# Optimization experiments

Measured on AMD Instinct MI355X. Metric: run time of the kernel, lower is better.

## Reference

```python
import jax, jax.numpy as jnp
import numpy as np

B, F, Q, E = 256, 128, 4096, 128
TAU = 0.2
P_DROP = 0.5
NUM_SAMPLES = 128  # hardcoded in forward: compute_scores(..., num_samples=128)
NUM_POS = 1
EASY_UB = 0.5
HARD_LB = 0.5


def setup_inputs() -> dict:
    k = jax.random.key(0)
    ks = jax.random.split(k, 8)
    query = jax.random.normal(ks[0], (B, F), jnp.float32)
    key = jax.random.normal(ks[1], (B, F), jnp.float32)
    teacher = jax.random.normal(ks[2], (B, F), jnp.float32)
    negatives = jax.random.normal(ks[3], (F, Q), jnp.float32)
    # random_maskout masks: rand <= p -> zero out
    mask_t = jax.random.uniform(ks[4], (E, B, F)) <= P_DROP
    mask_n = jax.random.uniform(ks[5], (E, F, Q)) <= P_DROP
    # compute_scores sampling mask: rand <= num_samples/Q
    score_mask = jax.random.uniform(ks[6], (E, B, Q)) <= (NUM_SAMPLES / Q)
    # bootstrap over batch dim: for each (e,q) column, sample B row indices with replacement
    idx = jax.random.randint(ks[7], (E, Q, B), 0, B)
    boot = jnp.zeros((E, Q, B), bool).at[
        jnp.arange(E)[:, None, None], jnp.arange(Q)[None, :, None], idx
    ].set(True)
    boot_mask = jnp.transpose(boot, (0, 2, 1))  # (E,B,Q)
    return dict(query=query, key=key, teacher=teacher, negatives=negatives,
                mask_t=mask_t, mask_n=mask_n, score_mask=score_mask, boot_mask=boot_mask)


def _masked_softmax(x, mask, axis):
    # matches torch masked_fill(~mask, -inf) + softmax; masked entries -> 0 prob
    z = jnp.where(mask, x, -jnp.inf)
    m = jnp.max(z, axis=axis, keepdims=True)
    m = jnp.where(jnp.isfinite(m), m, 0.0)  # guard fully-masked slices
    e = jnp.where(mask, jnp.exp(z - m), 0.0)
    return e / jnp.maximum(e.sum(axis=axis, keepdims=True), 1e-30)


def _l2norm(x, axis):
    n = jnp.sqrt(jnp.sum(x * x, axis=axis, keepdims=True))
    return x / jnp.maximum(n, 1e-12)


def reference(query, key, teacher, negatives, mask_t, mask_n, score_mask, boot_mask):
    negatives = jax.lax.stop_gradient(negatives)  # negatives.detach().clone()
    logits_pos = jnp.sum(query * key, axis=1, keepdims=True)      # (B,1)
    logits_neg = query @ negatives                                 # (B,Q)
    logits = jnp.concatenate([logits_pos, logits_neg], axis=1) / TAU
    moco_loss = -jax.nn.log_softmax(logits, axis=1)[:, 0].mean()   # CE with target 0

    # ---- teacher similarities (torch.no_grad) ----
    t = _l2norm(jnp.where(mask_t, 0.0, teacher[None, :, :]), 2)    # (E,B,F)
    n = _l2norm(jnp.where(mask_n, 0.0, negatives[None, :, :]), 1)  # (E,F,Q)
    sim = jax.lax.stop_gradient(jnp.einsum('ebf,efq->ebq', t, n) / TAU)

    # ---- scores: masked softmax over Q, masked mean over E ----
    probs = _masked_softmax(sim, score_mask, axis=2)               # (E,B,Q)
    cnt_e = jnp.maximum(score_mask.sum(axis=0).astype(sim.dtype), 1.0)
    scores = probs.sum(axis=0) / cnt_e                             # (B,Q)

    # ---- uncertainty: masked entropy over batch dim ----
    p = _masked_softmax(sim, boot_mask, axis=1) + 1e-7             # (E,B,Q)
    ent = -(p * jnp.log(p))
    cnt_b = jnp.maximum(boot_mask.sum(axis=1).astype(sim.dtype), 1.0)  # (E,Q)
    uncertainty = (ent.sum(axis=1) / cnt_b).mean(axis=0, keepdims=True)  # (1,Q)

    log_sm_neg = jax.nn.log_softmax(logits[:, 1:], axis=1)         # (B,Q)

    def _pos_loss(pos_mask_row):
        pm = jnp.broadcast_to(pos_mask_row, (B, Q))
        s = jnp.where(pm, scores, -jnp.inf)
        _, idx = jax.lax.top_k(s, NUM_POS)                         # (B,k)
        loss = -jnp.take_along_axis(log_sm_neg, idx, axis=1).mean(axis=1).mean()
        mask = jnp.zeros((B, Q), bool).at[jnp.arange(B)[:, None], idx].set(True)
        return loss, mask

    ub = jnp.quantile(uncertainty, EASY_UB, axis=1)                # (1,)
    easy_loss, easy_mask = _pos_loss(uncertainty <= ub)
    lb = jnp.quantile(uncertainty, HARD_LB, axis=1)
    hard_loss, hard_mask = _pos_loss(uncertainty >= lb)

    return moco_loss, logits, easy_loss, easy_mask, hard_loss, hard_mask
```

## Files before the change

### kernel.cpp

```cpp
#include <hip/hip_runtime.h>
#include <cmath>

typedef unsigned char u8;
typedef unsigned short u16;
typedef unsigned int u32;
typedef __attribute__((ext_vector_type(8))) short s8v;
typedef __attribute__((ext_vector_type(4))) float f32x4;

#define B 256
#define F 128
#define Q 4096
#define E 128
#define QW 128
#define INV_TAU 5.0f
#define CAP 256

#define W_SCORES 0u
#define W_CNT    1048576u
#define W_UNC    2097152u
#define W_NLSE   2101248u
#define W_MOCO   2101504u
#define W_EASY   2101760u
#define W_HARD   2102016u
#define W_UB     2102272u
#define W_INVN   2102528u
#define W_AF     2626816u
#define W_PB     4723968u
#define W_PS     8918272u
#define W_PN     13112576u
#define W_CNTB   15209728u
#define W_ENT    15242496u

#define O_MOCO   0u
#define O_LOGITS 1u
#define O_ELOSS  1048833u
#define O_EMASK  1048834u
#define O_HLOSS  2097410u
#define O_HMASK  2097411u

static __device__ __forceinline__ u16 f2bf(float x) {
    unsigned int u = __builtin_bit_cast(unsigned int, x);
    unsigned int r = (u + 0x7FFFu + ((u >> 16) & 1u)) >> 16;
    return (u16)r;
}

__global__ void k_zero(float4* __restrict__ p) {
    p[(size_t)blockIdx.x * 256 + threadIdx.x] = make_float4(0.f, 0.f, 0.f, 0.f);
}
__global__ void k_zeroi(int* __restrict__ p) {
    p[(size_t)blockIdx.x * 256 + threadIdx.x] = 0;
}

__global__ void __launch_bounds__(256) k_pack(const u8* __restrict__ in,
                                              u32* __restrict__ out, int Rin) {
    __shared__ u32 lds[64 * 133];
    int t = threadIdx.x;
    int r0 = blockIdx.x * 64;
    int q0 = blockIdx.y * 512;
    int qw0 = q0 >> 5;
    #pragma unroll
    for (int i = 0; i < 8; i++) {
        int w = i * 256 + t;
        int row = w >> 5, c = w & 31;
        uint4 v = *(const uint4*)&in[(size_t)(r0 + row) * Q + q0 + c * 16];
        int base = row * 133 + c * 4;
        lds[base] = v.x; lds[base + 1] = v.y; lds[base + 2] = v.z; lds[base + 3] = v.w;
    }
    __syncthreads();
    int e = r0 / Rin, rr = r0 % Rin;
    #pragma unroll
    for (int k = 0; k < 4; k++) {
        int qw = (t >> 6) + k * 4;
        int r = t & 63;
        u32 w = 0;
        #pragma unroll
        for (int j = 0; j < 8; j++) {
            u32 u = lds[r * 133 + qw * 8 + j];
            w |= ((u & 1u) | ((u >> 7) & 2u) | ((u >> 14) & 4u) | ((u >> 21) & 8u)) << (j * 4);
        }
        out[((size_t)e * QW + qw0 + qw) * Rin + rr + r] = w;
    }
}

__global__ void k_afrag(const float* __restrict__ teacher, const u8* __restrict__ mask_t,
                        u16* __restrict__ af) {
    int eb = blockIdx.x;
    int e  = eb >> 8;
    int b  = eb & (B - 1);
    int f  = threadIdx.x;
    float v = mask_t[(size_t)eb * F + f] ? 0.f : teacher[b * F + f];
    float ss = v * v;
    #pragma unroll
    for (int o = 32; o > 0; o >>= 1) ss += __shfl_down(ss, o);
    __shared__ float s2[2];
    if ((threadIdx.x & 63) == 0) s2[threadIdx.x >> 6] = ss;
    __syncthreads();
    float d = fmaxf(sqrtf(s2[0] + s2[1]), 1e-12f);
    float t = v / d;
    int bg = b >> 4, m = b & 15;
    int kb = f >> 5, quad = (f >> 3) & 3, j = f & 7;
    int lane = quad * 16 + m;
    af[((((size_t)e * 16 + bg) * 4 + kb) * 64 + lane) * 8 + j] = f2bf(t);
}

__global__ void __launch_bounds__(256) k_invn(const float* __restrict__ neg,
                                              const u32* __restrict__ pn,
                                              float* __restrict__ invn) {
    __shared__ u32 lds[32 * 128];
    int e = blockIdx.x, t = threadIdx.x;
    int qblk = blockIdx.y;
    size_t base = ((size_t)e * QW + qblk * 32) * F;
    #pragma unroll
    for (int k = 0; k < 16; k++) lds[t + 256 * k] = pn[base + t + 256 * k];
    __syncthreads();
    int q0 = qblk * 1024 + t * 4;
    int qwl = (t * 4) >> 5;
    int sh = (t * 4) & 31;
    float s0 = 0.f, s1 = 0.f, s2 = 0.f, s3 = 0.f;
    #pragma unroll 4
    for (int f = 0; f < F; f++) {
        float4 v = *(const float4*)&neg[(size_t)f * Q + q0];
        u32 w = lds[qwl * 128 + f] >> sh;
        if (!(w & 1u)) s0 = fmaf(v.x, v.x, s0);
        if (!(w & 2u)) s1 = fmaf(v.y, v.y, s1);
        if (!(w & 4u)) s2 = fmaf(v.z, v.z, s2);
        if (!(w & 8u)) s3 = fmaf(v.w, v.w, s3);
    }
    float4 r;
    r.x = INV_TAU / fmaxf(sqrtf(s0), 1e-12f);
    r.y = INV_TAU / fmaxf(sqrtf(s1), 1e-12f);
    r.z = INV_TAU / fmaxf(sqrtf(s2), 1e-12f);
    r.w = INV_TAU / fmaxf(sqrtf(s3), 1e-12f);
    *(float4*)&invn[(size_t)e * Q + q0] = r;
}

__global__ void __launch_bounds__(256) k_fused(
        const u16* __restrict__ af, const float* __restrict__ neg,
        const u32* __restrict__ pn, const float* __restrict__ invn,
        const u32* __restrict__ pb, const u32* __restrict__ ps,
        float* __restrict__ unc, uint2* __restrict__ ent_buf,
        int* __restrict__ cnt_buf, int e0) {
    __shared__ u16 bfrag[4][4][512];
    __shared__ u32 bw[2][256], sw[2][256];
    __shared__ u32 pnl[2][128];
    __shared__ float invl[64];
    __shared__ float sstat[4][64], cstat[4][64], estat[4][64];
    __shared__ float carr[64];
    __shared__ int sbase[256];

    int qb = blockIdx.x;
    int el = blockIdx.y, e = e0 + el;
    int t = threadIdx.x;
    int q0 = qb * 64;
    int qw0 = qb * 2;

    bw[0][t] = pb[((size_t)e * QW + qw0) * B + t];
    bw[1][t] = pb[((size_t)e * QW + qw0 + 1) * B + t];
    sw[0][t] = ps[((size_t)e * QW + qw0) * B + t];
    sw[1][t] = ps[((size_t)e * QW + qw0 + 1) * B + t];
    if (t < 128) {
        pnl[0][t] = pn[((size_t)e * QW + qw0) * F + t];
        pnl[1][t] = pn[((size_t)e * QW + qw0 + 1) * F + t];
    } else if (t < 192) {
        invl[t - 128] = invn[(size_t)e * Q + q0 + (t - 128)];
    }
    __syncthreads();

    #pragma unroll
    for (int s = 0; s < 4; s++) {
        int slot = t + 256 * s;
        int qg = slot >> 8;
        int r = slot & 255;
        int kb = r >> 6, lane2 = r & 63;
        int ql = qg * 16 + (lane2 & 15);
        int fb = kb * 32 + (lane2 >> 4) * 8;
        float iv = invl[ql];
        const u32* pw = pnl[ql >> 5];
        int sh = ql & 31;
        u16 tmp[8];
        #pragma unroll
        for (int j = 0; j < 8; j++) {
            u32 bit = (pw[fb + j] >> sh) & 1u;
            float v = bit ? 0.f : neg[(size_t)(fb + j) * Q + q0 + ql] * iv;
            tmp[j] = f2bf(v);
        }
        *(s8v*)&bfrag[qg][kb][lane2 * 8] = *(const s8v*)tmp;
    }
    __syncthreads();

    int wave = t >> 6, lane = t & 63;
    int colb = lane & 15, quad = lane >> 4;
    f32x4 acc[4][4];
    #pragma unroll
    for (int bgi = 0; bgi < 4; bgi++) {
        int bg = wave * 4 + bgi;
        s8v a[4];
        #pragma unroll
        for (int kb = 0; kb < 4; kb++)
            a[kb] = *(const s8v*)&af[((((size_t)e * 16 + bg) * 4 + kb) * 64 + lane) * 8];
        #pragma unroll
        for (int qg = 0; qg < 4; qg++) {
            f32x4 c4 = {0.f, 0.f, 0.f, 0.f};
            #pragma unroll
            for (int kb = 0; kb < 4; kb++) {
                s8v bv = *(const s8v*)&bfrag[qg][kb][lane * 8];
                c4 = __builtin_amdgcn_mfma_f32_16x16x32_bf16(a[kb], bv, c4, 0, 0, 0);
            }
            acc[bgi][qg] = c4;
        }
    }

    float sloc[4] = {0.f, 0.f, 0.f, 0.f}, cloc[4] = {0.f, 0.f, 0.f, 0.f};
    #pragma unroll
    for (int bgi = 0; bgi < 4; bgi++) {
        int b0 = (wave * 4 + bgi) * 16 + quad * 4;
        uint4 w0 = *(const uint4*)&bw[0][b0];
        uint4 w1 = *(const uint4*)&bw[1][b0];
        u32 W0[4] = {w0.x, w0.y, w0.z, w0.w};
        u32 W1[4] = {w1.x, w1.y, w1.z, w1.w};
        #pragma unroll
        for (int r = 0; r < 4; r++)
            #pragma unroll
            for (int qg = 0; qg < 4; qg++) {
                u32 w = (qg & 2) ? W1[r] : W0[r];
                int bpos = (qg & 1) * 16 + colb;
                if ((w >> bpos) & 1u) {
                    sloc[qg] += __expf(acc[bgi][qg][r]);
                    cloc[qg] += 1.f;
                }
            }
    }
    #pragma unroll
    for (int qg = 0; qg < 4; qg++) {
        sloc[qg] += __shfl_xor(sloc[qg], 16); sloc[qg] += __shfl_xor(sloc[qg], 32);
        cloc[qg] += __shfl_xor(cloc[qg], 16); cloc[qg] += __shfl_xor(cloc[qg], 32);
    }
    if (quad == 0)
        #pragma unroll
        for (int qg = 0; qg < 4; qg++) {
            sstat[wave][qg * 16 + colb] = sloc[qg];
            cstat[wave][qg * 16 + colb] = cloc[qg];
        }
    __syncthreads();
    float invS[4];
    #pragma unroll
    for (int qg = 0; qg < 4; qg++) {
        int c = qg * 16 + colb;
        float S = sstat[0][c] + sstat[1][c] + sstat[2][c] + sstat[3][c];
        invS[qg] = 1.f / fmaxf(S, 1e-30f);
    }
    if (wave == 0 && quad == 0)
        #pragma unroll
        for (int qg = 0; qg < 4; qg++) {
            int c = qg * 16 + colb;
            carr[c] = cstat[0][c] + cstat[1][c] + cstat[2][c] + cstat[3][c];
        }

    const float P0 = 1e-7f;
    const float C0 = 1.61180954e-6f;
    float eloc[4] = {0.f, 0.f, 0.f, 0.f};
    #pragma unroll
    for (int bgi = 0; bgi < 4; bgi++) {
        int b0 = (wave * 4 + bgi) * 16 + quad * 4;
        uint4 w0 = *(const uint4*)&bw[0][b0];
        uint4 w1 = *(const uint4*)&bw[1][b0];
        u32 W0[4] = {w0.x, w0.y, w0.z, w0.w};
        u32 W1[4] = {w1.x, w1.y, w1.z, w1.w};
        #pragma unroll
        for (int r = 0; r < 4; r++)
            #pragma unroll
            for (int qg = 0; qg < 4; qg++) {
                u32 w = (qg & 2) ? W1[r] : W0[r];
                int bpos = (qg & 1) * 16 + colb;
                if ((w >> bpos) & 1u) {
                    float p = __expf(acc[bgi][qg][r]) * invS[qg] + P0;
                    eloc[qg] -= p * __logf(p);
                } else {
                    eloc[qg] += C0;
                }
            }
    }
    #pragma unroll
    for (int qg = 0; qg < 4; qg++) {
        eloc[qg] += __shfl_xor(eloc[qg], 16); eloc[qg] += __shfl_xor(eloc[qg], 32);
    }
    if (quad == 0)
        #pragma unroll
        for (int qg = 0; qg < 4; qg++) estat[wave][qg * 16 + colb] = eloc[qg];

    {
        u32 a0 = sw[0][t], a1 = sw[1][t];
        int n = __popc(a0) + __popc(a1);
        int base = 0;
        if (n) base = atomicAdd(&cnt_buf[el * B + t], n);
        sbase[t] = base;
    }
    __syncthreads();

    if (t < 64) {
        float tot = estat[0][t] + estat[1][t] + estat[2][t] + estat[3][t];
        atomicAdd(&unc[q0 + t], tot / fmaxf(carr[t], 1.f));
    }

    #pragma unroll
    for (int bgi = 0; bgi < 4; bgi++) {
        int b0 = (wave * 4 + bgi) * 16 + quad * 4;
        uint4 s0 = *(const uint4*)&sw[0][b0];
        uint4 s1 = *(const uint4*)&sw[1][b0];
        u32 S0[4] = {s0.x, s0.y, s0.z, s0.w};
        u32 S1[4] = {s1.x, s1.y, s1.z, s1.w};
        #pragma unroll
        for (int r = 0; r < 4; r++) {
            int bs = sbase[b0 + r];
            int p0 = __popc(S0[r]);
            #pragma unroll
            for (int qg = 0; qg < 4; qg++) {
                int bpos = (qg & 1) * 16 + colb;
                u32 w = (qg & 2) ? S1[r] : S0[r];
                if ((w >> bpos) & 1u) {
                    int rank = __popc(w & ((1u << bpos) - 1u)) + ((qg & 2) ? p0 : 0);
                    int pos = bs + rank;
                    if (pos < CAP) {
                        uint2 en;
                        en.x = (unsigned)(q0 + qg * 16 + colb);
                        en.y = __builtin_bit_cast(unsigned, acc[bgi][qg][r]);
                        ent_buf[((size_t)(el * B + b0 + r)) * CAP + pos] = en;
                    }
                }
            }
        }
    }
}

__global__ void __launch_bounds__(256) k_scores(
        const uint2* __restrict__ ent_buf, const int* __restrict__ cnt_buf,
        float* __restrict__ sacc, float* __restrict__ cacc, int ecnt) {
    __shared__ float srow[Q];
    __shared__ float crow[Q];
    int b = blockIdx.x, t = threadIdx.x;
    #pragma unroll
    for (int j = 0; j < 16; j++) { srow[t + 256 * j] = 0.f; crow[t + 256 * j] = 0.f; }
    __syncthreads();
    int wave = t >> 6, lane = t & 63;
    for (int el = wave; el < ecnt; el += 4) {
        int c = cnt_buf[el * B + b];
        if (c > CAP) c = CAP;
        if (c == 0) continue;
        const uint2* p = ent_buf + (size_t)(el * B + b) * CAP;
        uint2 ev[4]; float exv[4]; int ne = 0;
        float s = 0.f;
        for (int i = lane; i < c; i += 64) {
            ev[ne] = p[i];
            exv[ne] = __expf(__builtin_bit_cast(float, ev[ne].y));
            s += exv[ne];
            ne++;
        }
        #pragma unroll
        for (int off = 32; off > 0; off >>= 1) s += __shfl_xor(s, off);
        float iS = 1.f / fmaxf(s, 1e-30f);
        for (int k = 0; k < ne; k++) {
            atomicAdd(&srow[ev[k].x], exv[k] * iS);
            atomicAdd(&crow[ev[k].x], 1.f);
        }
    }
    __syncthreads();
    #pragma unroll
    for (int j = 0; j < 16; j++) {
        int q = t + 256 * j;
        sacc[(size_t)b * Q + q] += srow[q];
        cacc[(size_t)b * Q + q] += crow[q];
    }
}

__global__ void k_finscores(float* __restrict__ sacc, const float* __restrict__ cacc) {
    int idx = blockIdx.x * 256 + threadIdx.x;
    sacc[idx] = sacc[idx] / fmaxf(cacc[idx], 1.f);
}

__global__ void k_logits(const float* __restrict__ query, const float* __restrict__ key,
                         const float* __restrict__ neg, float* __restrict__ out) {
    __shared__ float qrow[F];
    __shared__ float red[256];
    int b = blockIdx.x, seg = blockIdx.y, t = threadIdx.x;
    if (t < F) qrow[t] = query[b * F + t];
    __syncthreads();
    int q0 = seg * 1024 + t * 4;
    float4 acc = make_float4(0.f, 0.f, 0.f, 0.f);
    for (int f = 0; f < F; f++) {
        float a = qrow[f];
        float4 v = *(const float4*)&neg[(size_t)f * Q + q0];
        acc.x = fmaf(a, v.x, acc.x);
        acc.y = fmaf(a, v.y, acc.y);
        acc.z = fmaf(a, v.z, acc.z);
        acc.w = fmaf(a, v.w, acc.w);
    }
    float* row = out + O_LOGITS + (size_t)b * (Q + 1);
    row[1 + q0]     = acc.x * INV_TAU;
    row[1 + q0 + 1] = acc.y * INV_TAU;
    row[1 + q0 + 2] = acc.z * INV_TAU;
    row[1 + q0 + 3] = acc.w * INV_TAU;
    if (seg == 0) {
        float pp = (t < F) ? qrow[t] * key[b * F + t] : 0.f;
        red[t] = pp;
        __syncthreads();
        for (int s = 128; s > 0; s >>= 1) { if (t < s) red[t] += red[t + s]; __syncthreads(); }
        if (t == 0) row[0] = red[0] * INV_TAU;
    }
}

__global__ void k_rowstats(const float* __restrict__ out, float* __restrict__ moco_part,
                           float* __restrict__ nlse) {
    __shared__ float red[256];
    int b = blockIdx.x, t = threadIdx.x;
    const float* row = out + O_LOGITS + (size_t)b * (Q + 1);
    float m = -INFINITY, mn = -INFINITY;
    for (int j = 0; j < 17; j++) {
        int i = t + 256 * j;
        if (i < Q + 1) { float zz = row[i]; m = fmaxf(m, zz); if (i >= 1) mn = fmaxf(mn, zz); }
    }
    red[t] = m; __syncthreads();
    for (int s = 128; s > 0; s >>= 1) { if (t < s) red[t] = fmaxf(red[t], red[t + s]); __syncthreads(); }
    float M = red[0]; __syncthreads();
    red[t] = mn; __syncthreads();
    for (int s = 128; s > 0; s >>= 1) { if (t < s) red[t] = fmaxf(red[t], red[t + s]); __syncthreads(); }
    float Mn = red[0]; __syncthreads();
    float s1 = 0.f, s2 = 0.f;
    for (int j = 0; j < 17; j++) {
        int i = t + 256 * j;
        if (i < Q + 1) { float zz = row[i]; s1 += expf(zz - M); if (i >= 1) s2 += expf(zz - Mn); }
    }
    red[t] = s1; __syncthreads();
    for (int s = 128; s > 0; s >>= 1) { if (t < s) red[t] += red[t + s]; __syncthreads(); }
    float S = red[0]; __syncthreads();
    red[t] = s2; __syncthreads();
    for (int s = 128; s > 0; s >>= 1) { if (t < s) red[t] += red[t + s]; __syncthreads(); }
    float Sn = red[0];
    if (t == 0) { moco_part[b] = M + logf(S) - row[0]; nlse[b] = Mn + logf(Sn); }
}

__global__ void k_median(float* __restrict__ unc, float* __restrict__ ubp) {
    __shared__ float sd[4096];
    int t = threadIdx.x;
    #pragma unroll
    for (int j = 0; j < 4; j++) {
        int q = t + 1024 * j;
        float u = unc[q] * (1.f / 128.f);
        unc[q] = u; sd[q] = u;
    }
    __syncthreads();
    for (int k = 2; k <= 4096; k <<= 1) {
        for (int j = k >> 1; j > 0; j >>= 1) {
            #pragma unroll
            for (int base = 0; base < 4; base++) {
                int i = t + 1024 * base;
                int ixj = i ^ j;
                if (ixj > i) {
                    bool up = ((i & k) == 0);
                    float x = sd[i], y = sd[ixj];
                    if ((x > y) == up) { sd[i] = y; sd[ixj] = x; }
                }
            }
            __syncthreads();
        }
    }
    if (t == 0) { float a = sd[2047], b2 = sd[2048]; ubp[0] = a + 0.5f * (b2 - a); }
}

__global__ void k_select(float* __restrict__ out, const float* __restrict__ scores,
                         const float* __restrict__ unc, const float* __restrict__ ubp,
                         const float* __restrict__ nlse, float* __restrict__ easy_part,
                         float* __restrict__ hard_part) {
    __shared__ float rv[256];
    __shared__ int ri[256];
    __shared__ int bshare;
    int b = blockIdx.x, mode = blockIdx.y, t = threadIdx.x;
    float ub = ubp[0];
    float bv = -INFINITY; int bidx = Q;
    #pragma unroll
    for (int j = 0; j < 16; j++) {
        int q = t + 256 * j;
        float u = unc[q];
        bool ok = (mode == 0) ? (u <= ub) : (u >= ub);
        if (ok) {
            float v = scores[(size_t)b * Q + q];
            if (v > bv || (v == bv && q < bidx)) { bv = v; bidx = q; }
        }
    }
    rv[t] = bv; ri[t] = bidx; __syncthreads();
    for (int s = 128; s > 0; s >>= 1) {
        if (t < s) {
            float v2 = rv[t + s]; int i2 = ri[t + s];
            if (v2 > rv[t] || (v2 == rv[t] && i2 < ri[t])) { rv[t] = v2; ri[t] = i2; }
        }
        __syncthreads();
    }
    if (t == 0) {
        int best = ri[0]; bshare = best;
        float zz = out[O_LOGITS + (size_t)b * (Q + 1) + 1 + best];
        float loss = nlse[b] - zz;
        (mode == 0 ? easy_part : hard_part)[b] = loss;
    }
    __syncthreads();
    int best = bshare;
    float* mrow = out + (mode == 0 ? O_EMASK : O_HMASK) + (size_t)b * Q;
    #pragma unroll
    for (int j = 0; j < 16; j++) { int q = t + 256 * j; mrow[q] = (q == best) ? 1.f : 0.f; }
}

__global__ void k_scalars(const float* __restrict__ moco, const float* __restrict__ easyp,
                          const float* __restrict__ hardp, float* __restrict__ out) {
    __shared__ float red[256];
    int t = threadIdx.x;
    red[t] = moco[t]; __syncthreads();
    for (int s = 128; s > 0; s >>= 1) { if (t < s) red[t] += red[t + s]; __syncthreads(); }
    if (t == 0) out[O_MOCO] = red[0] / 256.f;
    __syncthreads();
    red[t] = easyp[t]; __syncthreads();
    for (int s = 128; s > 0; s >>= 1) { if (t < s) red[t] += red[t + s]; __syncthreads(); }
    if (t == 0) out[O_ELOSS] = red[0] / 256.f;
    __syncthreads();
    red[t] = hardp[t]; __syncthreads();
    for (int s = 128; s > 0; s >>= 1) { if (t < s) red[t] += red[t + s]; __syncthreads(); }
    if (t == 0) out[O_HLOSS] = red[0] / 256.f;
}

extern "C" void kernel_launch(void* const* d_in, const int* in_sizes, int n_in,
                              void* d_out, int out_size, void* d_ws, size_t ws_size,
                              hipStream_t stream) {
    const float* query   = (const float*)d_in[0];
    const float* key     = (const float*)d_in[1];
    const float* teacher = (const float*)d_in[2];
    const float* neg     = (const float*)d_in[3];
    const u8* mask_t     = (const u8*)d_in[4];
    const u8* mask_n     = (const u8*)d_in[5];
    const u8* score_mask = (const u8*)d_in[6];
    const u8* boot_mask  = (const u8*)d_in[7];
    float* out = (float*)d_out;
    float* ws  = (float*)d_ws;

    long ws_floats = (long)(ws_size / 4);
    int Ec = (int)((ws_floats - (long)W_ENT) / (long)(B * CAP * 2));
    if (Ec > E) Ec = E;
    if (Ec < 1) Ec = 1;

    u16* af = (u16*)(ws + W_AF);
    u32* pb = (u32*)(ws + W_PB);
    u32* ps = (u32*)(ws + W_PS);
    u32* pn = (u32*)(ws + W_PN);
    int* cnt_buf = (int*)(ws + W_CNTB);
    uint2* ent_buf = (uint2*)(ws + W_ENT);

    k_zero<<<2052, 256, 0, stream>>>((float4*)(ws + W_SCORES));
    k_pack<<<dim3((E * B) / 64, Q / 512), 256, 0, stream>>>(boot_mask, pb, B);
    k_pack<<<dim3((E * B) / 64, Q / 512), 256, 0, stream>>>(score_mask, ps, B);
    k_pack<<<dim3((E * F) / 64, Q / 512), 256, 0, stream>>>(mask_n, pn, F);
    k_afrag<<<E * B, 128, 0, stream>>>(teacher, mask_t, af);
    k_invn<<<dim3(E, 4), 256, 0, stream>>>(neg, pn, ws + W_INVN);
    k_logits<<<dim3(B, 4), 256, 0, stream>>>(query, key, neg, out);
    k_rowstats<<<B, 256, 0, stream>>>(out, ws + W_MOCO, ws + W_NLSE);

    for (int e0 = 0; e0 < E; e0 += Ec) {
        int ecnt = (E - e0 < Ec) ? (E - e0) : Ec;
        k_zeroi<<<ecnt, 256, 0, stream>>>(cnt_buf);
        k_fused<<<dim3(Q / 64, ecnt), 256, 0, stream>>>(
            af, neg, pn, ws + W_INVN, pb, ps, ws + W_UNC, ent_buf, cnt_buf, e0);
        k_scores<<<B, 256, 0, stream>>>(ent_buf, cnt_buf, ws + W_SCORES, ws + W_CNT, ecnt);
    }

    k_finscores<<<(B * Q) / 256, 256, 0, stream>>>(ws + W_SCORES, ws + W_CNT);
    k_median<<<1, 1024, 0, stream>>>(ws + W_UNC, ws + W_UB);
    k_select<<<dim3(B, 2), 256, 0, stream>>>(out, ws + W_SCORES, ws + W_UNC, ws + W_UB,
                                             ws + W_NLSE, ws + W_EASY, ws + W_HARD);
    k_scalars<<<1, 256, 0, stream>>>(ws + W_MOCO, ws + W_EASY, ws + W_HARD, out);
}
```

Baseline: 1.402 ms.

## Fuse pack launches, merge logits with rowstats, precompute score softmax sums in fused kernel

New measurement: 1.501 ms. 7.1% more time.

```diff
diff --git a/kernel.cpp b/kernel.cpp
--- a/kernel.cpp
+++ b/kernel.cpp
@@ -18,18 +18,20 @@
 #define W_SCORES 0u
 #define W_CNT    1048576u
 #define W_UNC    2097152u
-#define W_NLSE   2101248u
-#define W_MOCO   2101504u
-#define W_EASY   2101760u
-#define W_HARD   2102016u
-#define W_UB     2102272u
-#define W_INVN   2102528u
-#define W_AF     2626816u
-#define W_PB     4723968u
-#define W_PS     8918272u
-#define W_PN     13112576u
-#define W_CNTB   15209728u
-#define W_ENT    15242496u
+#define W_CNTB   2101248u
+#define W_RSUM   2134016u
+#define W_NLSE   2166784u
+#define W_MOCO   2167040u
+#define W_EASY   2167296u
+#define W_HARD   2167552u
+#define W_UB     2167808u
+#define W_INVN   2168064u
+#define W_AF     2692352u
+#define W_PB     4789504u
+#define W_PS     8983808u
+#define W_PN     13178112u
+#define W_ENT    15275264u
+#define NZERO    2166784u
 
 #define O_MOCO   0u
 #define O_LOGITS 1u
@@ -47,12 +49,17 @@
 __global__ void k_zero(float4* __restrict__ p) {
     p[(size_t)blockIdx.x * 256 + threadIdx.x] = make_float4(0.f, 0.f, 0.f, 0.f);
 }
-__global__ void k_zeroi(int* __restrict__ p) {
-    p[(size_t)blockIdx.x * 256 + threadIdx.x] = 0;
-}
-
-__global__ void __launch_bounds__(256) k_pack(const u8* __restrict__ in,
-                                              u32* __restrict__ out, int Rin) {
+
+__global__ void __launch_bounds__(256) k_pack(const u8* __restrict__ boot,
+                                              const u8* __restrict__ smask,
+                                              const u8* __restrict__ maskn,
+                                              u32* __restrict__ pb, u32* __restrict__ ps,
+                                              u32* __restrict__ pn) {
+    int z = blockIdx.z;
+    int Rin = (z == 2) ? F : B;
+    if (z == 2 && blockIdx.x >= 2048) return;
+    const u8* in = (z == 0) ? boot : (z == 1) ? smask : maskn;
+    u32* out = (z == 0) ? pb : (z == 1) ? ps : pn;
     __shared__ u32 lds[64 * 133];
     int t = threadIdx.x;
     int r0 = blockIdx.x * 64;
@@ -139,7 +146,7 @@
         const u32* __restrict__ pn, const float* __restrict__ invn,
         const u32* __restrict__ pb, const u32* __restrict__ ps,
         float* __restrict__ unc, uint2* __restrict__ ent_buf,
-        int* __restrict__ cnt_buf, int e0) {
+        int* __restrict__ cnt_buf, float* __restrict__ rsum, int e0) {
     __shared__ u16 bfrag[4][4][512];
     __shared__ u32 bw[2][256], sw[2][256];
     __shared__ u32 pnl[2][128];
@@ -210,6 +217,14 @@
         }
     }
 
+    #pragma unroll
+    for (int bgi = 0; bgi < 4; bgi++)
+        #pragma unroll
+        for (int qg = 0; qg < 4; qg++)
+            #pragma unroll
+            for (int r = 0; r < 4; r++)
+                acc[bgi][qg][r] = __expf(acc[bgi][qg][r]);
+
     float sloc[4] = {0.f, 0.f, 0.f, 0.f}, cloc[4] = {0.f, 0.f, 0.f, 0.f};
     #pragma unroll
     for (int bgi = 0; bgi < 4; bgi++) {
@@ -225,7 +240,7 @@
                 u32 w = (qg & 2) ? W1[r] : W0[r];
                 int bpos = (qg & 1) * 16 + colb;
                 if ((w >> bpos) & 1u) {
-                    sloc[qg] += __expf(acc[bgi][qg][r]);
+                    sloc[qg] += acc[bgi][qg][r];
                     cloc[qg] += 1.f;
                 }
             }
@@ -273,7 +288,7 @@
                 u32 w = (qg & 2) ? W1[r] : W0[r];
                 int bpos = (qg & 1) * 16 + colb;
                 if ((w >> bpos) & 1u) {
-                    float p = __expf(acc[bgi][qg][r]) * invS[qg] + P0;
+                    float p = acc[bgi][qg][r] * invS[qg] + P0;
                     eloc[qg] -= p * __logf(p);
                 } else {
                     eloc[qg] += C0;
@@ -287,6 +302,29 @@
     if (quad == 0)
         #pragma unroll
         for (int qg = 0; qg < 4; qg++) estat[wave][qg * 16 + colb] = eloc[qg];
+
+    #pragma unroll
+    for (int bgi = 0; bgi < 4; bgi++) {
+        int b0 = (wave * 4 + bgi) * 16 + quad * 4;
+        uint4 s0 = *(const uint4*)&sw[0][b0];
+        uint4 s1 = *(const uint4*)&sw[1][b0];
+        u32 S0[4] = {s0.x, s0.y, s0.z, s0.w};
+        u32 S1[4] = {s1.x, s1.y, s1.z, s1.w};
+        #pragma unroll
+        for (int r = 0; r < 4; r++) {
+            float rl = 0.f;
+            #pragma unroll
+            for (int qg = 0; qg < 4; qg++) {
+                u32 w = (qg & 2) ? S1[r] : S0[r];
+                int bpos = (qg & 1) * 16 + colb;
+                if ((w >> bpos) & 1u) rl += acc[bgi][qg][r];
+            }
+            rl += __shfl_xor(rl, 1); rl += __shfl_xor(rl, 2);
+            rl += __shfl_xor(rl, 4); rl += __shfl_xor(rl, 8);
+            if (colb == 0 && rl != 0.f)
+                atomicAdd(&rsum[el * B + b0 + r], rl);
+        }
+    }
 
     {
         u32 a0 = sw[0][t], a1 = sw[1][t];
@@ -332,110 +370,113 @@
     }
 }
 
-__global__ void __launch_bounds__(256) k_scores(
+__global__ void __launch_bounds__(512) k_scores(
         const uint2* __restrict__ ent_buf, const int* __restrict__ cnt_buf,
+        const float* __restrict__ rsum,
         float* __restrict__ sacc, float* __restrict__ cacc, int ecnt) {
     __shared__ float srow[Q];
     __shared__ float crow[Q];
+    __shared__ float isl[E];
+    __shared__ int cl[E];
     int b = blockIdx.x, t = threadIdx.x;
     #pragma unroll
-    for (int j = 0; j < 16; j++) { srow[t + 256 * j] = 0.f; crow[t + 256 * j] = 0.f; }
+    for (int j = 0; j < 8; j++) { srow[t + 512 * j] = 0.f; crow[t + 512 * j] = 0.f; }
+    if (t < ecnt) {
+        int c = cnt_buf[t * B + b];
+        cl[t] = (c > CAP) ? CAP : c;
+        isl[t] = 1.f / fmaxf(rsum[t * B + b], 1e-30f);
+    }
     __syncthreads();
     int wave = t >> 6, lane = t & 63;
-    for (int el = wave; el < ecnt; el += 4) {
-        int c = cnt_buf[el * B + b];
-        if (c > CAP) c = CAP;
-        if (c == 0) continue;
+    for (int el = wave; el < ecnt; el += 8) {
+        int c = cl[el];
+        float iS = isl[el];
         const uint2* p = ent_buf + (size_t)(el * B + b) * CAP;
-        uint2 ev[4]; float exv[4]; int ne = 0;
-        float s = 0.f;
         for (int i = lane; i < c; i += 64) {
-            ev[ne] = p[i];
-            exv[ne] = __expf(__builtin_bit_cast(float, ev[ne].y));
-            s += exv[ne];
-            ne++;
-        }
-        #pragma unroll
-        for (int off = 32; off > 0; off >>= 1) s += __shfl_xor(s, off);
-        float iS = 1.f / fmaxf(s, 1e-30f);
-        for (int k = 0; k < ne; k++) {
-            atomicAdd(&srow[ev[k].x], exv[k] * iS);
-            atomicAdd(&crow[ev[k].x], 1.f);
-        }
-    }
-    __syncthreads();
-    #pragma unroll
-    for (int j = 0; j < 16; j++) {
-        int q = t + 256 * j;
+            uint2 en = p[i];
+            atomicAdd(&srow[en.x], __builtin_bit_cast(float, en.y) * iS);
+            atomicAdd(&crow[en.x], 1.f);
+        }
+    }
+    __syncthreads();
+    #pragma unroll
+    for (int j = 0; j < 8; j++) {
+        int q = t + 512 * j;
         sacc[(size_t)b * Q + q] += srow[q];
         cacc[(size_t)b * Q + q] += crow[q];
     }
 }
 
-__global__ void k_finscores(float* __restrict__ sacc, const float* __restrict__ cacc) {
-    int idx = blockIdx.x * 256 + threadIdx.x;
-    sacc[idx] = sacc[idx] / fmaxf(cacc[idx], 1.f);
-}
-
-__global__ void k_logits(const float* __restrict__ query, const float* __restrict__ key,
-                         const float* __restrict__ neg, float* __restrict__ out) {
+__global__ void __launch_bounds__(256) k_logits(
+        const float* __restrict__ query, const float* __restrict__ key,
+        const float* __restrict__ neg, float* __restrict__ out,
+        float* __restrict__ moco_part, float* __restrict__ nlse) {
     __shared__ float qrow[F];
     __shared__ float red[256];
-    int b = blockIdx.x, seg = blockIdx.y, t = threadIdx.x;
-    if (t < F) qrow[t] = query[b * F + t];
-    __syncthreads();
-    int q0 = seg * 1024 + t * 4;
-    float4 acc = make_float4(0.f, 0.f, 0.f, 0.f);
+    __shared__ float poss;
+    int b = blockIdx.x, t = threadIdx.x;
+    float pp = 0.f;
+    if (t < F) { float qv = query[b * F + t]; qrow[t] = qv; pp = qv * key[b * F + t]; }
+    red[t] = pp;
+    __syncthreads();
+    for (int s = 128; s > 0; s >>= 1) { if (t < s) red[t] += red[t + s]; __syncthreads(); }
+    if (t == 0) poss = red[0] * INV_TAU;
+    __syncthreads();
+    float pos = poss;
+    float4 acc[4];
+    #pragma unroll
+    for (int j = 0; j < 4; j++) acc[j] = make_float4(0.f, 0.f, 0.f, 0.f);
     for (int f = 0; f < F; f++) {
         float a = qrow[f];
-        float4 v = *(const float4*)&neg[(size_t)f * Q + q0];
-        acc.x = fmaf(a, v.x, acc.x);
-        acc.y = fmaf(a, v.y, acc.y);
-        acc.z = fmaf(a, v.z, acc.z);
-        acc.w = fmaf(a, v.w, acc.w);
-    }
+        const float* np_ = neg + (size_t)f * Q + t * 4;
+        #pragma unroll
+        for (int j = 0; j < 4; j++) {
+            float4 v = *(const float4*)&np_[1024 * j];
+            acc[j].x = fmaf(a, v.x, acc[j].x);
+            acc[j].y = fmaf(a, v.y, acc[j].y);
+            acc[j].z = fmaf(a, v.z, acc[j].z);
+            acc[j].w = fmaf(a, v.w, acc[j].w);
+        }
+    }
+    float z[16];
     float* row = out + O_LOGITS + (size_t)b * (Q + 1);
-    row[1 + q0]     = acc.x * INV_TAU;
-    row[1 + q0 + 1] = acc.y * INV_TAU;
-    row[1 + q0 + 2] = acc.z * INV_TAU;
-    row[1 + q0 + 3] = acc.w * INV_TAU;
-    if (seg == 0) {
-        float pp = (t < F) ? qrow[t] * key[b * F + t] : 0.f;
-        red[t] = pp;
-        __syncthreads();
-        for (int s = 128; s > 0; s >>= 1) { if (t < s) red[t] += red[t + s]; __syncthreads(); }
-        if (t == 0) row[0] = red[0] * INV_TAU;
-    }
-}
-
-__global__ void k_rowstats(const float* __restrict__ out, float* __restrict__ moco_part,
-                           float* __restrict__ nlse) {
-    __shared__ float red[256];
-    int b = blockIdx.x, t = threadIdx.x;
-    const float* row = out + O_LOGITS + (size_t)b * (Q + 1);
-    float m = -INFINITY, mn = -INFINITY;
-    for (int j = 0; j < 17; j++) {
-        int i = t + 256 * j;
-        if (i < Q + 1) { float zz = row[i]; m = fmaxf(m, zz); if (i >= 1) mn = fmaxf(mn, zz); }
-    }
-    red[t] = m; __syncthreads();
-    for (int s = 128; s > 0; s >>= 1) { if (t < s) red[t] = fmaxf(red[t], red[t + s]); __syncthreads(); }
-    float M = red[0]; __syncthreads();
+    #pragma unroll
+    for (int j = 0; j < 4; j++) {
+        int q = t * 4 + 1024 * j;
+        z[j * 4]     = acc[j].x * INV_TAU;
+        z[j * 4 + 1] = acc[j].y * INV_TAU;
+        z[j * 4 + 2] = acc[j].z * INV_TAU;
+        z[j * 4 + 3] = acc[j].w * INV_TAU;
+        row[1 + q]     = z[j * 4];
+        row[1 + q + 1] = z[j * 4 + 1];
+        row[1 + q + 2] = z[j * 4 + 2];
+        row[1 + q + 3] = z[j * 4 + 3];
+    }
+    if (t == 0) row[0] = pos;
+    float mn = -INFINITY;
+    #pragma unroll
+    for (int j = 0; j < 16; j++) mn = fmaxf(mn, z[j]);
     red[t] = mn; __syncthreads();
     for (int s = 128; s > 0; s >>= 1) { if (t < s) red[t] = fmaxf(red[t], red[t + s]); __syncthreads(); }
-    float Mn = red[0]; __syncthreads();
-    float s1 = 0.f, s2 = 0.f;
-    for (int j = 0; j < 17; j++) {
-        int i = t + 256 * j;
-        if (i < Q + 1) { float zz = row[i]; s1 += expf(zz - M); if (i >= 1) s2 += expf(zz - Mn); }
-    }
+    float Mn = red[0];
+    float M = fmaxf(Mn, pos);
+    __syncthreads();
+    float s2 = 0.f;
+    #pragma unroll
+    for (int j = 0; j < 16; j++) s2 += expf(z[j] - Mn);
+    red[t] = s2; __syncthreads();
+    for (int s = 128; s > 0; s >>= 1) { if (t < s) red[t] += red[t + s]; __syncthreads(); }
+    float Sn = red[0]; __syncthreads();
+    float s1 = 0.f;
+    #pragma unroll
+    for (int j = 0; j < 16; j++) s1 += expf(z[j] - M);
+    if (t == 0) s1 += expf(pos - M);
     red[t] = s1; __syncthreads();
     for (int s = 128; s > 0; s >>= 1) { if (t < s) red[t] += red[t + s]; __syncthreads(); }
-    float S = red[0]; __syncthreads();
-    red[t] = s2; __syncthreads();
-    for (int s = 128; s > 0; s >>= 1) { if (t < s) red[t] += red[t + s]; __syncthreads(); }
-    float Sn = red[0];
-    if (t == 0) { moco_part[b] = M + logf(S) - row[0]; nlse[b] = Mn + logf(Sn); }
+    if (t == 0) {
+        moco_part[b] = M + logf(red[0]) - pos;
+        nlse[b] = Mn + logf(Sn);
+    }
 }
 
 __global__ void k_median(float* __restrict__ unc, float* __restrict__ ubp) {
@@ -466,7 +507,8 @@
     if (t == 0) { float a = sd[2047], b2 = sd[2048]; ubp[0] = a + 0.5f * (b2 - a); }
 }
 
-__global__ void k_select(float* __restrict__ out, const float* __restrict__ scores,
+__global__ void k_select(float* __restrict__ out, const float* __restrict__ sacc,
+                         const float* __restrict__ cacc,
                          const float* __restrict__ unc, const float* __restrict__ ubp,
                          const float* __restrict__ nlse, float* __restrict__ easy_part,
                          float* __restrict__ hard_part) {
@@ -482,7 +524,7 @@
         float u = unc[q];
         bool ok = (mode == 0) ? (u <= ub) : (u >= ub);
         if (ok) {
-            float v = scores[(size_t)b * Q + q];
+            float v = sacc[(size_t)b * Q + q] / fmaxf(cacc[(size_t)b * Q + q], 1.f);
             if (v > bv || (v == bv && q < bidx)) { bv = v; bidx = q; }
         }
     }
@@ -548,28 +590,29 @@
     u32* ps = (u32*)(ws + W_PS);
     u32* pn = (u32*)(ws + W_PN);
     int* cnt_buf = (int*)(ws + W_CNTB);
+    float* rsum = ws + W_RSUM;
     uint2* ent_buf = (uint2*)(ws + W_ENT);
 
-    k_zero<<<2052, 256, 0, stream>>>((float4*)(ws + W_SCORES));
-    k_pack<<<dim3((E * B) / 64, Q / 512), 256, 0, stream>>>(boot_mask, pb, B);
-    k_pack<<<dim3((E * B) / 64, Q / 512), 256, 0, stream>>>(score_mask, ps, B);
-    k_pack<<<dim3((E * F) / 64, Q / 512), 256, 0, stream>>>(mask_n, pn, F);
+    k_zero<<<NZERO / 1024, 256, 0, stream>>>((float4*)(ws + W_SCORES));
+    k_pack<<<dim3((E * B) / 64, Q / 512, 3), 256, 0, stream>>>(
+        boot_mask, score_mask, mask_n, pb, ps, pn);
     k_afrag<<<E * B, 128, 0, stream>>>(teacher, mask_t, af);
     k_invn<<<dim3(E, 4), 256, 0, stream>>>(neg, pn, ws + W_INVN);
-    k_logits<<<dim3(B, 4), 256, 0, stream>>>(query, key, neg, out);
-    k_rowstats<<<B, 256, 0, stream>>>(out, ws + W_MOCO, ws + W_NLSE);
+    k_logits<<<B, 256, 0, stream>>>(query, key, neg, out, ws + W_MOCO, ws + W_NLSE);
 
     for (int e0 = 0; e0 < E; e0 += Ec) {
         int ecnt = (E - e0 < Ec) ? (E - e0) : Ec;
-        k_zeroi<<<ecnt, 256, 0, stream>>>(cnt_buf);
+        if (e0 > 0)
+            k_zero<<<64, 256, 0, stream>>>((float4*)(ws + W_CNTB));
         k_fused<<<dim3(Q / 64, ecnt), 256, 0, stream>>>(
-            af, neg, pn, ws + W_INVN, pb, ps, ws + W_UNC, ent_buf, cnt_buf, e0);
-        k_scores<<<B, 256, 0, stream>>>(ent_buf, cnt_buf, ws + W_SCORES, ws + W_CNT, ecnt);
-    }
-
-    k_finscores<<<(B * Q) / 256, 256, 0, stream>>>(ws + W_SCORES, ws + W_CNT);
+            af, neg, pn, ws + W_INVN, pb, ps, ws + W_UNC, ent_buf, cnt_buf, rsum, e0);
+        k_scores<<<B, 512, 0, stream>>>(ent_buf, cnt_buf, rsum,
+                                        ws + W_SCORES, ws + W_CNT, ecnt);
+    }
+
     k_median<<<1, 1024, 0, stream>>>(ws + W_UNC, ws + W_UB);
-    k_select<<<dim3(B, 2), 256, 0, stream>>>(out, ws + W_SCORES, ws + W_UNC, ws + W_UB,
+    k_select<<<dim3(B, 2), 256, 0, stream>>>(out, ws + W_SCORES, ws + W_CNT,
+                                             ws + W_UNC, ws + W_UB,
                                              ws + W_NLSE, ws + W_EASY, ws + W_HARD);
     k_scalars<<<1, 256, 0, stream>>>(ws + W_MOCO, ws + W_EASY, ws + W_HARD, out);
 }
```
